# Optimization experiments

Measured on AMD Instinct MI355X. Metric: run time of the kernel, lower is better.

## Reference

```python
import jax, jax.numpy as jnp
import numpy as np

B, T, U, NC, TD = 128, 256, 1024, 5000, 128


def setup_inputs() -> dict:
    key = jax.random.key(0)
    ks = jax.random.split(key, 8)
    g = lambda k, shape, s=0.05: jax.random.normal(k, shape, jnp.float32) * s
    return {
        "x": jax.random.normal(ks[0], (B, T, 5), jnp.float32),
        "ch": jax.random.randint(ks[1], (B, T), 0, NC, dtype=jnp.int32),
        "Wd": g(ks[2], (2, TD)),
        "bd": jnp.zeros((TD,), jnp.float32),
        "Ws": g(ks[3], (3, TD)),
        "bs": jnp.zeros((TD,), jnp.float32),
        "recurrent_kernel": g(ks[4], (U, 4 * U)),
        "kernel_c": g(ks[5], (NC, 4 * U)),
        "kernel_d": g(ks[6], (TD, 4 * U)),
        "kernel_s": g(ks[7], (TD, 4 * U)),
        "bias": jnp.zeros((4 * U,), jnp.float32),
    }


def reference(x, ch, Wd, bd, Ws, bs, recurrent_kernel, kernel_c, kernel_d, kernel_s, bias):
    u = recurrent_kernel.shape[0]
    Rzr = recurrent_kernel[:, : 2 * u]          # z and r recurrent weights, fused
    Rh = recurrent_kernel[:, 2 * u: 3 * u]      # candidate
    Ro = recurrent_kernel[:, 3 * u:]            # output gate

    def step(carry, inp):
        h, d_prev = carry                        # h: [B,U], d_prev: [B,2]
        xt, cht = inp                            # xt: [B,5], cht: [B]
        d = xt[:, :2] + d_prev                   # running d accumulator
        s = xt[:, 2:5]
        _d = jnp.tanh(d @ Wd + bd)               # [B,TD]
        _s = jnp.tanh(s @ Ws + bs)               # [B,TD]
        # one-hot @ kernel_c == row gather (same math, no one-hot expansion)
        base = kernel_c[cht] + _d @ kernel_d + _s @ kernel_s + bias  # [B,4U]
        zr = jax.nn.sigmoid(h @ Rzr + base[:, : 2 * u])
        z, r = zr[:, :u], zr[:, u:]
        hh = jnp.tanh((r * h) @ Rh + base[:, 2 * u: 3 * u])
        h_new = z * h + (1.0 - z) * hh
        o = jnp.tanh(h_new @ Ro + base[:, 3 * u:])
        return (h_new, d), o

    b = x.shape[0]
    h0 = jnp.zeros((b, u), x.dtype)
    d0 = jnp.zeros((b, 2), x.dtype)
    xs = (jnp.swapaxes(x, 0, 1), jnp.swapaxes(ch, 0, 1))  # time-major
    _, os = jax.lax.scan(step, (h0, d0), xs)              # os: [T,B,U]
    return jnp.swapaxes(os, 0, 1)                          # [B,T,U]
```

## Files before the change

kernel.cpp:

```cpp
#include <hip/hip_runtime.h>
#include <cstdint>
#include <cstddef>

typedef _Float16 f16;
typedef _Float16 f16x8 __attribute__((ext_vector_type(8)));
typedef float f32x4 __attribute__((ext_vector_type(4)));

#define T_  256
#define U_  1024

#define WS_FLA  0u
#define WS_FLB  1024u
#define WS_HHI  4096u
#define WS_RH   266240u
#define WS_WT   528384u
#define WS_KDT  8916992u
#define WS_KST  9965568u
#define WS_A    11014144u
#define WS_END  27791360u

#define L_STHI 0
#define L_ABUF 32768
#define L_EXCH 40960
#define L_Z    65920
#define L_LB   67968
#define L_PACK 84352
#define LDS_SZ 85376
#define EXT(kq,ch,q) (L_EXCH + (((kq)*2+(ch))*3+(q))*1040)

#define SPIN_BOUND 65536

#define MFMA16(a,b,c) __builtin_amdgcn_mfma_f32_16x16x32_f16((a),(b),(c),0,0,0)
__device__ __forceinline__ float sigm(float v) { return 1.0f / (1.0f + __expf(-v)); }
__device__ __forceinline__ void vwait0() { asm volatile("s_waitcnt vmcnt(0)" ::: "memory"); }

__device__ __forceinline__ void gload_x4(f16x8& d, const void* p) {
  asm volatile("global_load_dwordx4 %0, %1, off sc0 sc1" : "=&v"(d) : "v"(p));
}
__device__ __forceinline__ void gstore_x4(void* p, f16x8 v) {
  asm volatile("global_store_dwordx4 %0, %1, off sc0 sc1" :: "v"(p), "v"(v) : "memory");
}
__device__ __forceinline__ unsigned gload_flag(const unsigned* p) {
  unsigned v;
  asm volatile("global_load_dword %0, %1, off sc0 sc1\n\ts_waitcnt vmcnt(0)"
               : "=&v"(v) : "v"(p) : "memory");
  return v;
}
__device__ __forceinline__ void gstore_flag(unsigned* p, unsigned v) {
  asm volatile("global_store_dword %0, %1, off sc0 sc1" :: "v"(p), "v"(v) : "memory");
}
__device__ __forceinline__ void bar_wait(unsigned* flags, int rg, unsigned target, int tid) {
  if (tid < 64) {
    const unsigned* f = flags + rg * 32 + (tid & 31);
    int it = 0;
    while (gload_flag(f) < target && ++it < SPIN_BOUND) __builtin_amdgcn_s_sleep(1);
  }
  __builtin_amdgcn_fence(__ATOMIC_ACQUIRE, "workgroup");
  __syncthreads();
}

__global__ __launch_bounds__(256) void prep_kernel(const float* __restrict__ rk,
                                                   const float* __restrict__ kd,
                                                   const float* __restrict__ ks,
                                                   f16* __restrict__ wT,
                                                   f16* __restrict__ kdT,
                                                   f16* __restrict__ ksT) {
  size_t i = (size_t)blockIdx.x * 256 + threadIdx.x;
  if (i < 4194304u) {
    int k = (int)(i >> 12), n = (int)(i & 4095);
    wT[(size_t)n * 1024 + k] = (f16)rk[i];
  } else if (i < 4718592u) {
    size_t j = i - 4194304u;
    int k = (int)(j >> 12), n = (int)(j & 4095);
    kdT[(size_t)n * 128 + k] = (f16)kd[j];
  } else {
    size_t j = i - 4718592u;
    int k = (int)(j >> 12), n = (int)(j & 4095);
    ksT[(size_t)n * 128 + k] = (f16)ks[j];
  }
}

__global__ __launch_bounds__(64) void acum_kernel(const float* __restrict__ x,
    const float* __restrict__ Wd, const float* __restrict__ bd,
    const float* __restrict__ Ws, const float* __restrict__ bs,
    f16* __restrict__ A) {
  const int b = blockIdx.x, lane = threadIdx.x;
  float w0[4], w1[4], w2[4], bb[4];
  #pragma unroll
  for (int q = 0; q < 4; ++q) {
    int col = lane + 64 * q;
    if (col < 128) { w0[q] = Wd[col]; w1[q] = Wd[128 + col]; w2[q] = 0.f; bb[q] = bd[col]; }
    else { int c2 = col - 128; w0[q] = Ws[c2]; w1[q] = Ws[128 + c2]; w2[q] = Ws[256 + c2]; bb[q] = bs[c2]; }
  }
  float d0 = 0.f, d1 = 0.f;
  for (int t = 0; t < T_; ++t) {
    const float* xp = x + ((size_t)b * T_ + t) * 5;
    float x0 = xp[0], x1 = xp[1], x2 = xp[2], x3 = xp[3], x4 = xp[4];
    d0 += x0; d1 += x1;
    f16* Ap = A + ((size_t)b * T_ + t) * 256;
    #pragma unroll
    for (int q = 0; q < 4; ++q) {
      int col = lane + 64 * q;
      float v = (col < 128) ? tanhf(d0 * w0[q] + d1 * w1[q] + bb[q])
                            : tanhf(x2 * w0[q] + x3 * w1[q] + x4 * w2[q] + bb[q]);
      Ap[col] = (f16)v;
    }
  }
}

__global__ __launch_bounds__(512) void sgru_kernel(
    const int* __restrict__ chp, const float* __restrict__ kcp,
    const float* __restrict__ bias, char* __restrict__ wsb,
    float* __restrict__ out) {
  extern __shared__ char lds[];
  const int tid  = threadIdx.x;
  const int wid  = tid >> 6;
  const int lane = tid & 63;
  const int lcol = lane & 15;
  const int kc   = lane >> 4;
  const int lin  = blockIdx.x;
  const int rg   = lin >> 5;
  const int c    = lin & 31;
  const int row0 = rg * 16;
  const int kq   = wid >> 1;
  const int chh  = wid & 1;
  const int rp = tid & 255, rm = rp >> 4, rl = rp & 15, rch = tid >> 8;
  const int rucol = 32 * c + 16 * rch + rl;
  const int wreg = wid >> 1, wch = wid & 1;
  const int bcolw = wreg * 1024 + 32 * c + 16 * wch + lcol;

  const f16* __restrict__ wT  = (const f16*)(wsb + WS_WT);
  const f16* __restrict__ kdT = (const f16*)(wsb + WS_KDT);
  const f16* __restrict__ ksT = (const f16*)(wsb + WS_KST);
  const f16* __restrict__ Ap  = (const f16*)(wsb + WS_A);
  unsigned* flagsA = (unsigned*)(wsb + WS_FLA);
  unsigned* flagsB = (unsigned*)(wsb + WS_FLB);

  f16x8 Bp1[3][8], BpB[8];
  #pragma unroll
  for (int q = 0; q < 3; ++q) {
    const int orig = (q == 2 ? 3072 : q * 1024) + 32 * c + 16 * chh + lcol;
    const f16* wp = wT + (size_t)orig * 1024;
    #pragma unroll
    for (int j = 0; j < 8; ++j)
      Bp1[q][j] = *(const f16x8*)(wp + (kq * 8 + j) * 32 + kc * 8);
  }
  #pragma unroll
  for (int j = 0; j < 8; ++j)
    BpB[j] = (j < 4) ? *(const f16x8*)(kdT + (size_t)bcolw * 128 + j * 32 + kc * 8)
                     : *(const f16x8*)(ksT + (size_t)bcolw * 128 + (j - 4) * 32 + kc * 8);
  const float biasv = bias[bcolw];
  float h_own = 0.f;
  int chreg[4]; float kcv[4];

  {
    f16x8 av = *(const f16x8*)(Ap + ((size_t)(row0 + (tid >> 5)) * T_ + 0) * 256 + (tid & 31) * 8);
    *(f16x8*)(lds + L_ABUF + (tid >> 5) * 512 + (((tid & 31) * 16) ^ (((tid >> 5) & 7) << 4))) = av;
  }
  #pragma unroll
  for (int e = 0; e < 4; ++e) {
    const size_t r = (size_t)(row0 + kc * 4 + e) * T_;
    kcv[e] = kcp[(size_t)chp[r] * 4096 + bcolw];
    chreg[e] = chp[r + 1];
  }
  __syncthreads();
  {
    f32x4 ab = {0.f, 0.f, 0.f, 0.f};
    #pragma unroll
    for (int j = 0; j < 8; ++j) {
      f16x8 a = *(f16x8*)(lds + L_ABUF + lcol * 512 + ((j * 64 + kc * 16) ^ ((lcol & 7) << 4)));
      ab = MFMA16(a, BpB[j], ab);
    }
    float* lb0 = (float*)(lds + L_LB);
    #pragma unroll
    for (int e = 0; e < 4; ++e)
      lb0[((kc * 4 + e) * 4 + wreg) * 32 + 16 * wch + lcol] = ab[e] + kcv[e] + biasv;
  }
  __syncthreads();

  for (int t = 0; ; ++t) {
    const int p = t & 1;
    float* LBp = (float*)(lds + L_LB + p * 8192);
    float* LBq = (float*)(lds + L_LB + (p ^ 1) * 8192);

    f16x8 sh[4];
    {
      const char* pH = wsb + WS_HHI + (size_t)row0 * 2048;
      #pragma unroll
      for (int it = 0; it < 4; ++it) gload_x4(sh[it], pH + it * 8192 + tid * 16);
    }
    const bool havA = (t + 1 < T_);
    f16x8 av;
    if (havA) {
      av = *(const f16x8*)(Ap + ((size_t)(row0 + (tid >> 5)) * T_ + (t + 1)) * 256 + (tid & 31) * 8);
      #pragma unroll
      for (int e = 0; e < 4; ++e) kcv[e] = kcp[(size_t)chreg[e] * 4096 + bcolw];
      if (t + 2 < T_) {
        #pragma unroll
        for (int e = 0; e < 4; ++e)
          chreg[e] = chp[(size_t)(row0 + kc * 4 + e) * T_ + (t + 2)];
      }
    }
    vwait0();
    #pragma unroll
    for (int it = 0; it < 4; ++it) {
      const int g = it * 8192 + tid * 16;
      const int r = g >> 11, cb = g & 2047;
      *(f16x8*)(lds + L_STHI + r * 2048 + (cb ^ ((r & 7) << 4))) = sh[it];
    }
    if (havA)
      *(f16x8*)(lds + L_ABUF + (tid >> 5) * 512 + (((tid & 31) * 16) ^ (((tid >> 5) & 7) << 4))) = av;
    __syncthreads();

    f32x4 acc[3] = {{0,0,0,0},{0,0,0,0},{0,0,0,0}};
    {
      const int hb = lcol * 2048, hsw = (lcol & 7) << 4;
      #pragma unroll
      for (int j = 0; j < 8; ++j) {
        f16x8 a = *(f16x8*)(lds + L_STHI + hb + (((kq * 8 + j) * 64 + kc * 16) ^ hsw));
        #pragma unroll
        for (int q = 0; q < 3; ++q) acc[q] = MFMA16(a, Bp1[q][j], acc[q]);
      }
    }
    #pragma unroll
    for (int q = 0; q < 3; ++q)
      #pragma unroll
      for (int e = 0; e < 4; ++e)
        *(float*)(lds + EXT(kq, chh, q) + e * 260 + (kc * 16 + lcol) * 4) = acc[q][e];
    __syncthreads();

    float vz = 0.f, vr = 0.f, vo = 0.f;
    {
      const int off = (rm & 3) * 260 + ((rm >> 2) * 16 + rl) * 4;
      #pragma unroll
      for (int k2 = 0; k2 < 4; ++k2) {
        vz += *(float*)(lds + EXT(k2, rch, 0) + off);
        vr += *(float*)(lds + EXT(k2, rch, 1) + off);
        vo += *(float*)(lds + EXT(k2, rch, 2) + off);
      }
    }
    const float obase = LBq[(rm * 4 + 3) * 32 + 16 * rch + rl];
    if (t == T_) {
      out[((size_t)(row0 + rm) * T_ + (t - 1)) * U_ + rucol] = tanhf(vo + obase);
      break;
    }
    {
      ((float*)(lds + L_Z))[rm * 32 + 16 * rch + rl] =
          sigm(vz + LBp[(rm * 4 + 0) * 32 + 16 * rch + rl]);
      const float rv = sigm(vr + LBp[(rm * 4 + 1) * 32 + 16 * rch + rl]);
      const float hv = (float)*(f16*)(lds + L_STHI + rm * 2048 + ((2 * rucol) ^ ((rm & 7) << 4)));
      *(f16*)(lds + L_PACK + rm * 64 + (16 * rch + rl) * 2) = (f16)(rv * hv);
    }
    __syncthreads();
    if (wid == 0) {
      f16x8 pv = *(f16x8*)(lds + L_PACK + (lane >> 2) * 64 + (lane & 3) * 16);
      gstore_x4(wsb + WS_RH + (size_t)(row0 + (lane >> 2)) * 2048 + c * 64 + (lane & 3) * 16, pv);
      vwait0();
      if (lane == 0) gstore_flag(flagsA + lin, (unsigned)(t + 1));
    }
    if (t > 0) out[((size_t)(row0 + rm) * T_ + (t - 1)) * U_ + rucol] = tanhf(vo + obase);
    if (havA) {
      f32x4 ab = {0.f, 0.f, 0.f, 0.f};
      #pragma unroll
      for (int j = 0; j < 8; ++j) {
        f16x8 a = *(f16x8*)(lds + L_ABUF + lcol * 512 + ((j * 64 + kc * 16) ^ ((lcol & 7) << 4)));
        ab = MFMA16(a, BpB[j], ab);
      }
      #pragma unroll
      for (int e = 0; e < 4; ++e)
        LBq[((kc * 4 + e) * 4 + wreg) * 32 + 16 * wch + lcol] = ab[e] + kcv[e] + biasv;
    }
    bar_wait(flagsA, rg, (unsigned)(t + 1), tid);

    f16x8 sr[4], b2[8];
    {
      const char* pR = wsb + WS_RH + (size_t)row0 * 2048;
      #pragma unroll
      for (int it = 0; it < 4; ++it) gload_x4(sr[it], pR + it * 8192 + tid * 16);
      const f16* wp2 = wT + (size_t)(2048 + 32 * c + 16 * chh + lcol) * 1024;
      #pragma unroll
      for (int j = 0; j < 8; ++j) b2[j] = *(const f16x8*)(wp2 + (kq * 8 + j) * 32 + kc * 8);
    }
    vwait0();
    #pragma unroll
    for (int it = 0; it < 4; ++it) {
      const int g = it * 8192 + tid * 16;
      const int r = g >> 11, cb = g & 2047;
      *(f16x8*)(lds + L_STHI + r * 2048 + (cb ^ ((r & 7) << 4))) = sr[it];
    }
    __syncthreads();
    f32x4 a2 = {0.f, 0.f, 0.f, 0.f};
    {
      const int hb = lcol * 2048, hsw = (lcol & 7) << 4;
      #pragma unroll
      for (int j = 0; j < 8; ++j) {
        f16x8 a = *(f16x8*)(lds + L_STHI + hb + (((kq * 8 + j) * 64 + kc * 16) ^ hsw));
        a2 = MFMA16(a, b2[j], a2);
      }
    }
    #pragma unroll
    for (int e = 0; e < 4; ++e)
      *(float*)(lds + EXT(kq, chh, 0) + e * 260 + (kc * 16 + lcol) * 4) = a2[e];
    __syncthreads();
    {
      const int off = (rm & 3) * 260 + ((rm >> 2) * 16 + rl) * 4;
      float v = 0.f;
      #pragma unroll
      for (int k2 = 0; k2 < 4; ++k2) v += *(float*)(lds + EXT(k2, rch, 0) + off);
      const float hh = tanhf(v + LBp[(rm * 4 + 2) * 32 + 16 * rch + rl]);
      const float zv = ((float*)(lds + L_Z))[rm * 32 + 16 * rch + rl];
      h_own = zv * h_own + (1.f - zv) * hh;
      *(f16*)(lds + L_PACK + rm * 64 + (16 * rch + rl) * 2) = (f16)h_own;
    }
    __syncthreads();
    if (wid == 0) {
      f16x8 pv = *(f16x8*)(lds + L_PACK + (lane >> 2) * 64 + (lane & 3) * 16);
      gstore_x4(wsb + WS_HHI + (size_t)(row0 + (lane >> 2)) * 2048 + c * 64 + (lane & 3) * 16, pv);
      vwait0();
      if (lane == 0) gstore_flag(flagsB + lin, (unsigned)(t + 1));
    }
    bar_wait(flagsB, rg, (unsigned)(t + 1), tid);
  }
}

extern "C" void kernel_launch(void* const* d_in, const int* in_sizes, int n_in,
                              void* d_out, int out_size, void* d_ws, size_t ws_size,
                              hipStream_t stream) {
  const float* x    = (const float*)d_in[0];
  const int*   ch   = (const int*)d_in[1];
  const float* Wd   = (const float*)d_in[2];
  const float* bd_  = (const float*)d_in[3];
  const float* Ws   = (const float*)d_in[4];
  const float* bs_  = (const float*)d_in[5];
  const float* rk   = (const float*)d_in[6];
  const float* kc_  = (const float*)d_in[7];
  const float* kd   = (const float*)d_in[8];
  const float* ks   = (const float*)d_in[9];
  const float* bias = (const float*)d_in[10];
  char* wsb = (char*)d_ws;
  float* out = (float*)d_out;
  if (ws_size < (size_t)WS_END) return;

  hipMemsetAsync(wsb, 0, WS_WT, stream);
  prep_kernel<<<20480, 256, 0, stream>>>(rk, kd, ks,
      (f16*)(wsb + WS_WT), (f16*)(wsb + WS_KDT), (f16*)(wsb + WS_KST));
  acum_kernel<<<128, 64, 0, stream>>>(x, Wd, bd_, Ws, bs_, (f16*)(wsb + WS_A));
  hipFuncSetAttribute((const void*)sgru_kernel,
                      hipFuncAttributeMaxDynamicSharedMemorySize, LDS_SZ);
  sgru_kernel<<<256, 512, LDS_SZ, stream>>>(ch, kc_, bias, wsb, out);
}
```

Measured before the change: 2.321 ms.

## Replace flag barriers with parity-tagged data polling for cross-block sync

Removes the separate flag stores and spin barriers between blocks of a row group. Each published f16 value now carries the step parity in its low mantissa bit, and consumers re-load chunks until every element shows the expected tag. This cuts a store-wait, flag store and flag poll round trip from each of the two sync points per step, and lets the r*h loads be issued before the bias MFMA work. The cost is one bit of f16 precision, possible repeated polling traffic on data lines, and correctness that depends on each 16-byte store becoming visible all at once.

```diff
diff --git a/kernel.cpp b/kernel.cpp
--- a/kernel.cpp
+++ b/kernel.cpp
@@ -5,12 +5,11 @@
 typedef _Float16 f16;
 typedef _Float16 f16x8 __attribute__((ext_vector_type(8)));
 typedef float f32x4 __attribute__((ext_vector_type(4)));
+typedef unsigned u32x4 __attribute__((ext_vector_type(4)));
 
 #define T_  256
 #define U_  1024
 
-#define WS_FLA  0u
-#define WS_FLB  1024u
 #define WS_HHI  4096u
 #define WS_RH   266240u
 #define WS_WT   528384u
@@ -28,7 +27,7 @@
 #define LDS_SZ 85376
 #define EXT(kq,ch,q) (L_EXCH + (((kq)*2+(ch))*3+(q))*1040)
 
-#define SPIN_BOUND 65536
+#define POLL_BOUND (1 << 18)
 
 #define MFMA16(a,b,c) __builtin_amdgcn_mfma_f32_16x16x32_f16((a),(b),(c),0,0,0)
 __device__ __forceinline__ float sigm(float v) { return 1.0f / (1.0f + __expf(-v)); }
@@ -40,23 +39,15 @@
 __device__ __forceinline__ void gstore_x4(void* p, f16x8 v) {
   asm volatile("global_store_dwordx4 %0, %1, off sc0 sc1" :: "v"(p), "v"(v) : "memory");
 }
-__device__ __forceinline__ unsigned gload_flag(const unsigned* p) {
-  unsigned v;
-  asm volatile("global_load_dword %0, %1, off sc0 sc1\n\ts_waitcnt vmcnt(0)"
-               : "=&v"(v) : "v"(p) : "memory");
-  return v;
-}
-__device__ __forceinline__ void gstore_flag(unsigned* p, unsigned v) {
-  asm volatile("global_store_dword %0, %1, off sc0 sc1" :: "v"(p), "v"(v) : "memory");
-}
-__device__ __forceinline__ void bar_wait(unsigned* flags, int rg, unsigned target, int tid) {
-  if (tid < 64) {
-    const unsigned* f = flags + rg * 32 + (tid & 31);
-    int it = 0;
-    while (gload_flag(f) < target && ++it < SPIN_BOUND) __builtin_amdgcn_s_sleep(1);
-  }
-  __builtin_amdgcn_fence(__ATOMIC_ACQUIRE, "workgroup");
-  __syncthreads();
+__device__ __forceinline__ bool chunk_ok(f16x8 v, unsigned tag) {
+  u32x4 d = __builtin_bit_cast(u32x4, v);
+  if (tag) { unsigned a = d[0] & d[1] & d[2] & d[3]; return (a & 0x10001u) == 0x10001u; }
+  unsigned o = d[0] | d[1] | d[2] | d[3];
+  return (o & 0x10001u) == 0u;
+}
+__device__ __forceinline__ unsigned short tag16(float x, unsigned tag) {
+  unsigned short us = __builtin_bit_cast(unsigned short, (f16)x);
+  return (unsigned short)((us & 0xFFFEu) | tag);
 }
 
 __global__ __launch_bounds__(256) void prep_kernel(const float* __restrict__ rk,
@@ -133,8 +124,6 @@
   const f16* __restrict__ kdT = (const f16*)(wsb + WS_KDT);
   const f16* __restrict__ ksT = (const f16*)(wsb + WS_KST);
   const f16* __restrict__ Ap  = (const f16*)(wsb + WS_A);
-  unsigned* flagsA = (unsigned*)(wsb + WS_FLA);
-  unsigned* flagsB = (unsigned*)(wsb + WS_FLB);
 
   f16x8 Bp1[3][8], BpB[8];
   #pragma unroll
@@ -180,15 +169,15 @@
 
   for (int t = 0; ; ++t) {
     const int p = t & 1;
+    const unsigned htag = (unsigned)(t & 1);
+    const unsigned ntag = (unsigned)((t + 1) & 1);
     float* LBp = (float*)(lds + L_LB + p * 8192);
     float* LBq = (float*)(lds + L_LB + (p ^ 1) * 8192);
 
     f16x8 sh[4];
-    {
-      const char* pH = wsb + WS_HHI + (size_t)row0 * 2048;
-      #pragma unroll
-      for (int it = 0; it < 4; ++it) gload_x4(sh[it], pH + it * 8192 + tid * 16);
-    }
+    const char* pH = wsb + WS_HHI + (size_t)row0 * 2048;
+    #pragma unroll
+    for (int it = 0; it < 4; ++it) gload_x4(sh[it], pH + it * 8192 + tid * 16);
     const bool havA = (t + 1 < T_);
     f16x8 av;
     if (havA) {
@@ -201,7 +190,22 @@
           chreg[e] = chp[(size_t)(row0 + kc * 4 + e) * T_ + (t + 2)];
       }
     }
-    vwait0();
+    {
+      bool ok0 = false, ok1 = false, ok2 = false, ok3 = false;
+      for (int rounds = 0; ; ) {
+        vwait0();
+        ok0 = ok0 || chunk_ok(sh[0], htag);
+        ok1 = ok1 || chunk_ok(sh[1], htag);
+        ok2 = ok2 || chunk_ok(sh[2], htag);
+        ok3 = ok3 || chunk_ok(sh[3], htag);
+        if (ok0 & ok1 & ok2 & ok3) break;
+        if (++rounds >= POLL_BOUND) break;
+        if (!ok0) gload_x4(sh[0], pH + 0 * 8192 + tid * 16);
+        if (!ok1) gload_x4(sh[1], pH + 1 * 8192 + tid * 16);
+        if (!ok2) gload_x4(sh[2], pH + 2 * 8192 + tid * 16);
+        if (!ok3) gload_x4(sh[3], pH + 3 * 8192 + tid * 16);
+      }
+    }
     #pragma unroll
     for (int it = 0; it < 4; ++it) {
       const int g = it * 8192 + tid * 16;
@@ -249,14 +253,21 @@
           sigm(vz + LBp[(rm * 4 + 0) * 32 + 16 * rch + rl]);
       const float rv = sigm(vr + LBp[(rm * 4 + 1) * 32 + 16 * rch + rl]);
       const float hv = (float)*(f16*)(lds + L_STHI + rm * 2048 + ((2 * rucol) ^ ((rm & 7) << 4)));
-      *(f16*)(lds + L_PACK + rm * 64 + (16 * rch + rl) * 2) = (f16)(rv * hv);
+      *(unsigned short*)(lds + L_PACK + rm * 64 + (16 * rch + rl) * 2) = tag16(rv * hv, ntag);
     }
     __syncthreads();
     if (wid == 0) {
       f16x8 pv = *(f16x8*)(lds + L_PACK + (lane >> 2) * 64 + (lane & 3) * 16);
       gstore_x4(wsb + WS_RH + (size_t)(row0 + (lane >> 2)) * 2048 + c * 64 + (lane & 3) * 16, pv);
-      vwait0();
-      if (lane == 0) gstore_flag(flagsA + lin, (unsigned)(t + 1));
+    }
+    f16x8 sr[4], b2[8];
+    const char* pR = wsb + WS_RH + (size_t)row0 * 2048;
+    #pragma unroll
+    for (int it = 0; it < 4; ++it) gload_x4(sr[it], pR + it * 8192 + tid * 16);
+    {
+      const f16* wp2 = wT + (size_t)(2048 + 32 * c + 16 * chh + lcol) * 1024;
+      #pragma unroll
+      for (int j = 0; j < 8; ++j) b2[j] = *(const f16x8*)(wp2 + (kq * 8 + j) * 32 + kc * 8);
     }
     if (t > 0) out[((size_t)(row0 + rm) * T_ + (t - 1)) * U_ + rucol] = tanhf(vo + obase);
     if (havA) {
@@ -270,18 +281,22 @@
       for (int e = 0; e < 4; ++e)
         LBq[((kc * 4 + e) * 4 + wreg) * 32 + 16 * wch + lcol] = ab[e] + kcv[e] + biasv;
     }
-    bar_wait(flagsA, rg, (unsigned)(t + 1), tid);
-
-    f16x8 sr[4], b2[8];
-    {
-      const char* pR = wsb + WS_RH + (size_t)row0 * 2048;
-      #pragma unroll
-      for (int it = 0; it < 4; ++it) gload_x4(sr[it], pR + it * 8192 + tid * 16);
-      const f16* wp2 = wT + (size_t)(2048 + 32 * c + 16 * chh + lcol) * 1024;
-      #pragma unroll
-      for (int j = 0; j < 8; ++j) b2[j] = *(const f16x8*)(wp2 + (kq * 8 + j) * 32 + kc * 8);
-    }
-    vwait0();
+    {
+      bool ok0 = false, ok1 = false, ok2 = false, ok3 = false;
+      for (int rounds = 0; ; ) {
+        vwait0();
+        ok0 = ok0 || chunk_ok(sr[0], ntag);
+        ok1 = ok1 || chunk_ok(sr[1], ntag);
+        ok2 = ok2 || chunk_ok(sr[2], ntag);
+        ok3 = ok3 || chunk_ok(sr[3], ntag);
+        if (ok0 & ok1 & ok2 & ok3) break;
+        if (++rounds >= POLL_BOUND) break;
+        if (!ok0) gload_x4(sr[0], pR + 0 * 8192 + tid * 16);
+        if (!ok1) gload_x4(sr[1], pR + 1 * 8192 + tid * 16);
+        if (!ok2) gload_x4(sr[2], pR + 2 * 8192 + tid * 16);
+        if (!ok3) gload_x4(sr[3], pR + 3 * 8192 + tid * 16);
+      }
+    }
     #pragma unroll
     for (int it = 0; it < 4; ++it) {
       const int g = it * 8192 + tid * 16;
@@ -310,16 +325,13 @@
       const float hh = tanhf(v + LBp[(rm * 4 + 2) * 32 + 16 * rch + rl]);
       const float zv = ((float*)(lds + L_Z))[rm * 32 + 16 * rch + rl];
       h_own = zv * h_own + (1.f - zv) * hh;
-      *(f16*)(lds + L_PACK + rm * 64 + (16 * rch + rl) * 2) = (f16)h_own;
+      *(unsigned short*)(lds + L_PACK + rm * 64 + (16 * rch + rl) * 2) = tag16(h_own, ntag);
     }
     __syncthreads();
     if (wid == 0) {
       f16x8 pv = *(f16x8*)(lds + L_PACK + (lane >> 2) * 64 + (lane & 3) * 16);
       gstore_x4(wsb + WS_HHI + (size_t)(row0 + (lane >> 2)) * 2048 + c * 64 + (lane & 3) * 16, pv);
-      vwait0();
-      if (lane == 0) gstore_flag(flagsB + lin, (unsigned)(t + 1));
-    }
-    bar_wait(flagsB, rg, (unsigned)(t + 1), tid);
+    }
   }
 }
 
```

Measured after the change: 2.668 ms. 14.9% more time.

## Compute r-gate first to publish r*h early; keep candidate weights in registers

Applied to the files above, without the earlier changes.

Each step now computes only the r-gate matmul first, then publishes r*h and raises the cross-block flag before computing the z and o gate matmuls. This lets the z/o work and the next A-projection overlap the inter-block barrier wait. The candidate-gate weights (Bp2) are loaded into registers once instead of being reloaded from global memory every step, and the kernel_c gather add is deferred until after the barrier. In exchange register pressure rises (launch_bounds set to 512,2) and an extra __syncthreads is added per step.

```diff
diff --git a/kernel.cpp b/kernel.cpp
--- a/kernel.cpp
+++ b/kernel.cpp
@@ -108,7 +108,7 @@
   }
 }
 
-__global__ __launch_bounds__(512) void sgru_kernel(
+__global__ __launch_bounds__(512, 2) void sgru_kernel(
     const int* __restrict__ chp, const float* __restrict__ kcp,
     const float* __restrict__ bias, char* __restrict__ wsb,
     float* __restrict__ out) {
@@ -136,7 +136,7 @@
   unsigned* flagsA = (unsigned*)(wsb + WS_FLA);
   unsigned* flagsB = (unsigned*)(wsb + WS_FLB);
 
-  f16x8 Bp1[3][8], BpB[8];
+  f16x8 Bp1[3][8], Bp2[8], BpB[8];
   #pragma unroll
   for (int q = 0; q < 3; ++q) {
     const int orig = (q == 2 ? 3072 : q * 1024) + 32 * c + 16 * chh + lcol;
@@ -144,6 +144,11 @@
     #pragma unroll
     for (int j = 0; j < 8; ++j)
       Bp1[q][j] = *(const f16x8*)(wp + (kq * 8 + j) * 32 + kc * 8);
+  }
+  {
+    const f16* wp2 = wT + (size_t)(2048 + 32 * c + 16 * chh + lcol) * 1024;
+    #pragma unroll
+    for (int j = 0; j < 8; ++j) Bp2[j] = *(const f16x8*)(wp2 + (kq * 8 + j) * 32 + kc * 8);
   }
   #pragma unroll
   for (int j = 0; j < 8; ++j)
@@ -184,15 +189,72 @@
     float* LBq = (float*)(lds + L_LB + (p ^ 1) * 8192);
 
     f16x8 sh[4];
-    {
-      const char* pH = wsb + WS_HHI + (size_t)row0 * 2048;
-      #pragma unroll
-      for (int it = 0; it < 4; ++it) gload_x4(sh[it], pH + it * 8192 + tid * 16);
-    }
+    const char* pH = wsb + WS_HHI + (size_t)row0 * 2048;
+    #pragma unroll
+    for (int it = 0; it < 4; ++it) gload_x4(sh[it], pH + it * 8192 + tid * 16);
     const bool havA = (t + 1 < T_);
     f16x8 av;
+    if (havA)
+      av = *(const f16x8*)(Ap + ((size_t)(row0 + (tid >> 5)) * T_ + (t + 1)) * 256 + (tid & 31) * 8);
+    vwait0();
+    #pragma unroll
+    for (int it = 0; it < 4; ++it) {
+      const int g = it * 8192 + tid * 16;
+      const int r = g >> 11, cb = g & 2047;
+      *(f16x8*)(lds + L_STHI + r * 2048 + (cb ^ ((r & 7) << 4))) = sh[it];
+    }
+    __syncthreads();
+
+    if (t < T_) {
+      f32x4 accr = {0.f, 0.f, 0.f, 0.f};
+      {
+        const int hb = lcol * 2048, hsw = (lcol & 7) << 4;
+        #pragma unroll
+        for (int j = 0; j < 8; ++j) {
+          f16x8 a = *(f16x8*)(lds + L_STHI + hb + (((kq * 8 + j) * 64 + kc * 16) ^ hsw));
+          accr = MFMA16(a, Bp1[1][j], accr);
+        }
+      }
+      #pragma unroll
+      for (int e = 0; e < 4; ++e)
+        *(float*)(lds + EXT(kq, chh, 1) + e * 260 + (kc * 16 + lcol) * 4) = accr[e];
+      __syncthreads();
+      {
+        const int off = (rm & 3) * 260 + ((rm >> 2) * 16 + rl) * 4;
+        float vr = 0.f;
+        #pragma unroll
+        for (int k2 = 0; k2 < 4; ++k2) vr += *(float*)(lds + EXT(k2, rch, 1) + off);
+        const float rv = sigm(vr + LBp[(rm * 4 + 1) * 32 + 16 * rch + rl]);
+        const float hv = (float)*(f16*)(lds + L_STHI + rm * 2048 + ((2 * rucol) ^ ((rm & 7) << 4)));
+        *(f16*)(lds + L_PACK + rm * 64 + (16 * rch + rl) * 2) = (f16)(rv * hv);
+      }
+      __syncthreads();
+      if (wid == 0) {
+        f16x8 pv = *(f16x8*)(lds + L_PACK + (lane >> 2) * 64 + (lane & 3) * 16);
+        gstore_x4(wsb + WS_RH + (size_t)(row0 + (lane >> 2)) * 2048 + c * 64 + (lane & 3) * 16, pv);
+        vwait0();
+        if (lane == 0) gstore_flag(flagsA + lin, (unsigned)(t + 1));
+      }
+    }
+
+    f32x4 accz = {0.f, 0.f, 0.f, 0.f}, acco = {0.f, 0.f, 0.f, 0.f};
+    {
+      const int hb = lcol * 2048, hsw = (lcol & 7) << 4;
+      #pragma unroll
+      for (int j = 0; j < 8; ++j) {
+        f16x8 a = *(f16x8*)(lds + L_STHI + hb + (((kq * 8 + j) * 64 + kc * 16) ^ hsw));
+        if (t < T_) accz = MFMA16(a, Bp1[0][j], accz);
+        acco = MFMA16(a, Bp1[2][j], acco);
+      }
+    }
+    #pragma unroll
+    for (int e = 0; e < 4; ++e) {
+      if (t < T_)
+        *(float*)(lds + EXT(kq, chh, 0) + e * 260 + (kc * 16 + lcol) * 4) = accz[e];
+      *(float*)(lds + EXT(kq, chh, 2) + e * 260 + (kc * 16 + lcol) * 4) = acco[e];
+    }
     if (havA) {
-      av = *(const f16x8*)(Ap + ((size_t)(row0 + (tid >> 5)) * T_ + (t + 1)) * 256 + (tid & 31) * 8);
+      *(f16x8*)(lds + L_ABUF + (tid >> 5) * 512 + (((tid & 31) * 16) ^ (((tid >> 5) & 7) << 4))) = av;
       #pragma unroll
       for (int e = 0; e < 4; ++e) kcv[e] = kcp[(size_t)chreg[e] * 4096 + bcolw];
       if (t + 2 < T_) {
@@ -201,64 +263,23 @@
           chreg[e] = chp[(size_t)(row0 + kc * 4 + e) * T_ + (t + 2)];
       }
     }
-    vwait0();
-    #pragma unroll
-    for (int it = 0; it < 4; ++it) {
-      const int g = it * 8192 + tid * 16;
-      const int r = g >> 11, cb = g & 2047;
-      *(f16x8*)(lds + L_STHI + r * 2048 + (cb ^ ((r & 7) << 4))) = sh[it];
-    }
-    if (havA)
-      *(f16x8*)(lds + L_ABUF + (tid >> 5) * 512 + (((tid & 31) * 16) ^ (((tid >> 5) & 7) << 4))) = av;
-    __syncthreads();
-
-    f32x4 acc[3] = {{0,0,0,0},{0,0,0,0},{0,0,0,0}};
-    {
-      const int hb = lcol * 2048, hsw = (lcol & 7) << 4;
-      #pragma unroll
-      for (int j = 0; j < 8; ++j) {
-        f16x8 a = *(f16x8*)(lds + L_STHI + hb + (((kq * 8 + j) * 64 + kc * 16) ^ hsw));
-        #pragma unroll
-        for (int q = 0; q < 3; ++q) acc[q] = MFMA16(a, Bp1[q][j], acc[q]);
-      }
-    }
-    #pragma unroll
-    for (int q = 0; q < 3; ++q)
-      #pragma unroll
-      for (int e = 0; e < 4; ++e)
-        *(float*)(lds + EXT(kq, chh, q) + e * 260 + (kc * 16 + lcol) * 4) = acc[q][e];
-    __syncthreads();
-
-    float vz = 0.f, vr = 0.f, vo = 0.f;
+    __syncthreads();
     {
       const int off = (rm & 3) * 260 + ((rm >> 2) * 16 + rl) * 4;
+      float vz = 0.f, vo = 0.f;
       #pragma unroll
       for (int k2 = 0; k2 < 4; ++k2) {
-        vz += *(float*)(lds + EXT(k2, rch, 0) + off);
-        vr += *(float*)(lds + EXT(k2, rch, 1) + off);
+        if (t < T_) vz += *(float*)(lds + EXT(k2, rch, 0) + off);
         vo += *(float*)(lds + EXT(k2, rch, 2) + off);
       }
-    }
-    const float obase = LBq[(rm * 4 + 3) * 32 + 16 * rch + rl];
-    if (t == T_) {
-      out[((size_t)(row0 + rm) * T_ + (t - 1)) * U_ + rucol] = tanhf(vo + obase);
-      break;
-    }
-    {
-      ((float*)(lds + L_Z))[rm * 32 + 16 * rch + rl] =
-          sigm(vz + LBp[(rm * 4 + 0) * 32 + 16 * rch + rl]);
-      const float rv = sigm(vr + LBp[(rm * 4 + 1) * 32 + 16 * rch + rl]);
-      const float hv = (float)*(f16*)(lds + L_STHI + rm * 2048 + ((2 * rucol) ^ ((rm & 7) << 4)));
-      *(f16*)(lds + L_PACK + rm * 64 + (16 * rch + rl) * 2) = (f16)(rv * hv);
-    }
-    __syncthreads();
-    if (wid == 0) {
-      f16x8 pv = *(f16x8*)(lds + L_PACK + (lane >> 2) * 64 + (lane & 3) * 16);
-      gstore_x4(wsb + WS_RH + (size_t)(row0 + (lane >> 2)) * 2048 + c * 64 + (lane & 3) * 16, pv);
-      vwait0();
-      if (lane == 0) gstore_flag(flagsA + lin, (unsigned)(t + 1));
-    }
-    if (t > 0) out[((size_t)(row0 + rm) * T_ + (t - 1)) * U_ + rucol] = tanhf(vo + obase);
+      const float obase = LBq[(rm * 4 + 3) * 32 + 16 * rch + rl];
+      if (t > 0) out[((size_t)(row0 + rm) * T_ + (t - 1)) * U_ + rucol] = tanhf(vo + obase);
+      if (t < T_)
+        ((float*)(lds + L_Z))[rm * 32 + 16 * rch + rl] =
+            sigm(vz + LBp[(rm * 4 + 0) * 32 + 16 * rch + rl]);
+    }
+    if (t == T_) break;
+    __syncthreads();
     if (havA) {
       f32x4 ab = {0.f, 0.f, 0.f, 0.f};
       #pragma unroll
@@ -268,19 +289,14 @@
       }
       #pragma unroll
       for (int e = 0; e < 4; ++e)
-        LBq[((kc * 4 + e) * 4 + wreg) * 32 + 16 * wch + lcol] = ab[e] + kcv[e] + biasv;
+        LBq[((kc * 4 + e) * 4 + wreg) * 32 + 16 * wch + lcol] = ab[e] + biasv;
     }
     bar_wait(flagsA, rg, (unsigned)(t + 1), tid);
 
-    f16x8 sr[4], b2[8];
-    {
-      const char* pR = wsb + WS_RH + (size_t)row0 * 2048;
-      #pragma unroll
-      for (int it = 0; it < 4; ++it) gload_x4(sr[it], pR + it * 8192 + tid * 16);
-      const f16* wp2 = wT + (size_t)(2048 + 32 * c + 16 * chh + lcol) * 1024;
-      #pragma unroll
-      for (int j = 0; j < 8; ++j) b2[j] = *(const f16x8*)(wp2 + (kq * 8 + j) * 32 + kc * 8);
-    }
+    f16x8 sr[4];
+    const char* pR = wsb + WS_RH + (size_t)row0 * 2048;
+    #pragma unroll
+    for (int it = 0; it < 4; ++it) gload_x4(sr[it], pR + it * 8192 + tid * 16);
     vwait0();
     #pragma unroll
     for (int it = 0; it < 4; ++it) {
@@ -295,12 +311,17 @@
       #pragma unroll
       for (int j = 0; j < 8; ++j) {
         f16x8 a = *(f16x8*)(lds + L_STHI + hb + (((kq * 8 + j) * 64 + kc * 16) ^ hsw));
-        a2 = MFMA16(a, b2[j], a2);
+        a2 = MFMA16(a, Bp2[j], a2);
       }
     }
     #pragma unroll
     for (int e = 0; e < 4; ++e)
       *(float*)(lds + EXT(kq, chh, 0) + e * 260 + (kc * 16 + lcol) * 4) = a2[e];
+    if (havA) {
+      #pragma unroll
+      for (int e = 0; e < 4; ++e)
+        LBq[((kc * 4 + e) * 4 + wreg) * 32 + 16 * wch + lcol] += kcv[e];
+    }
     __syncthreads();
     {
       const int off = (rm & 3) * 260 + ((rm >> 2) * 16 + rl) * 4;
```

Measured after the change: 1.947 ms. -16.1%, faster.
